# Kernel tuning notes

Hardware: AMD Instinct MI355X
Metric: run time of the kernel (lower is better)

The kernel has to match this reference:

```python
import jax, jax.numpy as jnp
import numpy as np

B, H, W, D = 32, 56, 56, 192
WS, NH, SHIFT = 7, 6, 3
DH = D // NH          # head dim = 32
N = WS * WS           # 49 tokens per window
NW = (H // WS) * (W // WS)  # 64 windows per image
EPS = 1e-5


def _rel_pos_index():
    coords = np.stack(np.meshgrid(np.arange(WS), np.arange(WS), indexing='ij'))  # (2,WS,WS)
    flat = coords.reshape(2, -1)
    rel = flat[:, :, None] - flat[:, None, :]            # (2,N,N)
    rel = rel.transpose(1, 2, 0).astype(np.int64)        # (N,N,2)
    rel[..., 0] += WS - 1
    rel[..., 1] += WS - 1
    rel[..., 0] *= 2 * WS - 1
    return rel.sum(-1)                                    # (N,N) in [0,169)


def _shift_mask():
    img = np.zeros((H, W))
    bounds = [(0, H - WS), (H - WS, H - SHIFT), (H - SHIFT, H)]
    cnt = 0
    for h0, h1 in bounds:
        for w0, w1 in bounds:
            img[h0:h1, w0:w1] = cnt
            cnt += 1
    win = img.reshape(H // WS, WS, W // WS, WS).transpose(0, 2, 1, 3).reshape(-1, N)  # (nW,N)
    diff = win[:, None, :] - win[:, :, None]
    return np.where(diff != 0, -100.0, 0.0).astype(np.float32)  # (nW,N,N)


_REL_IDX = jnp.asarray(_rel_pos_index())
_MASK = jnp.asarray(_shift_mask())


def _layernorm(x, g, b):
    mu = jnp.mean(x, -1, keepdims=True)
    var = jnp.mean(jnp.square(x - mu), -1, keepdims=True)
    return (x - mu) * jax.lax.rsqrt(var + EPS) * g + b


def _window_partition(x):  # (B,H,W,C) -> (B*nW, N, C)
    Bx, _, _, C = x.shape
    x = x.reshape(Bx, H // WS, WS, W // WS, WS, C).transpose(0, 1, 3, 2, 4, 5)
    return x.reshape(-1, N, C)


def _window_reverse(w):  # (B*nW, N, C) -> (B,H,W,C)
    C = w.shape[-1]
    x = w.reshape(-1, H // WS, W // WS, WS, WS, C).transpose(0, 1, 3, 2, 4, 5)
    return x.reshape(-1, H, W, C)


def setup_inputs() -> dict:
    key = jax.random.key(0)
    ks = jax.random.split(key, 8)
    s = 0.02
    return {
        'x': jax.random.normal(ks[0], (B, H * W, D), jnp.float32),
        'norm1_g': jnp.ones((D,), jnp.float32),
        'norm1_b': jnp.zeros((D,), jnp.float32),
        'qkv_w': jax.random.normal(ks[1], (D, 3 * D), jnp.float32) * s,
        'qkv_b': jnp.zeros((3 * D,), jnp.float32),
        'proj_wo': jax.random.normal(ks[2], (D, D), jnp.float32) * s,
        'proj_bo': jnp.zeros((D,), jnp.float32),
        'rpb': jax.random.normal(ks[3], ((2 * WS - 1) ** 2, NH), jnp.float32) * s,
        'pl_w': jax.random.normal(ks[4], (NH, NH), jnp.float32) * s,
        'pl_b': jnp.zeros((NH,), jnp.float32),
        'pw_w': jax.random.normal(ks[5], (NH, NH), jnp.float32) * s,
        'pw_b': jnp.zeros((NH,), jnp.float32),
        'norm2_g': jnp.ones((D,), jnp.float32),
        'norm2_b': jnp.zeros((D,), jnp.float32),
        'fc1_w': jax.random.normal(ks[6], (D, 4 * D), jnp.float32) * s,
        'fc1_b': jnp.zeros((4 * D,), jnp.float32),
        'fc2_w': jax.random.normal(ks[7], (4 * D, D), jnp.float32) * s,
        'fc2_b': jnp.zeros((D,), jnp.float32),
    }


def reference(x, norm1_g, norm1_b, qkv_w, qkv_b, proj_wo, proj_bo, rpb,
              pl_w, pl_b, pw_w, pw_b, norm2_g, norm2_b,
              fc1_w, fc1_b, fc2_w, fc2_b):
    shortcut = x
    h = _layernorm(x, norm1_g, norm1_b).reshape(B, H, W, D)
    h = jnp.roll(h, (-SHIFT, -SHIFT), (1, 2))             # shifted windows
    win = _window_partition(h)                            # (B_, N, D), B_ = B*NW
    B_ = win.shape[0]

    qkv = win @ qkv_w + qkv_b                             # (B_, N, 3D)
    q_out, k_out, v_out = qkv[..., :D], qkv[..., D:2 * D], qkv[..., 2 * D:]
    qkv5 = qkv.reshape(B_, N, 3, NH, DH)
    q = qkv5[:, :, 0].transpose(0, 2, 1, 3)               # (B_, H, N, d)
    k = qkv5[:, :, 1].transpose(0, 2, 1, 3)
    v = qkv5[:, :, 2].transpose(0, 2, 1, 3)

    scale = DH ** -0.5
    attn = jnp.einsum('bhnd,bhmd->bhnm', q * scale, k)    # (B_, H, N, N)
    bias = rpb[_REL_IDX.reshape(-1)].reshape(N, N, NH).transpose(2, 0, 1)
    attn = attn + bias[None]
    # proj_l over the head axis (distillation transform, pre-softmax)
    attn = jnp.einsum('bhnm,hg->bgnm', attn, pl_w) + pl_b[None, :, None, None]
    # shifted-window mask
    attn = attn.reshape(B, NW, NH, N, N) + _MASK[None, :, None]
    attn = jax.nn.softmax(attn.reshape(B_, NH, N, N), axis=-1)
    # proj_w over the head axis (post-softmax)
    attn = jnp.einsum('bhnm,hg->bgnm', attn, pw_w) + pw_b[None, :, None, None]

    out = jnp.einsum('bhnm,bhmd->bnhd', attn, v).reshape(B_, N, D)
    out = out @ proj_wo + proj_bo

    h = _window_reverse(out)                              # (B,H,W,D)
    h = jnp.roll(h, (SHIFT, SHIFT), (1, 2)).reshape(B, H * W, D)
    xo = shortcut + h

    m = _layernorm(xo, norm2_g, norm2_b)
    m = jax.nn.gelu(m @ fc1_w + fc1_b, approximate=False) @ fc2_w + fc2_b
    xo = xo + m
    return xo, (q_out, k_out, v_out)
```

## Files before the change

kernel.cpp:

```cpp
#include <hip/hip_runtime.h>
#include <math.h>

#define TOK   100352
#define OUTCH 19267584L
#define NWIN  2048

typedef __attribute__((ext_vector_type(4))) float f32x4;
typedef __attribute__((ext_vector_type(8))) short bf16x8;

__device__ __forceinline__ unsigned short f2bf(float f) {
    unsigned u = __builtin_bit_cast(unsigned, f);
    u += 0x7FFFu + ((u >> 16) & 1u);
    return (unsigned short)(u >> 16);
}
__device__ __forceinline__ float bf2f(unsigned short s) {
    return __builtin_bit_cast(float, (unsigned)s << 16);
}

__global__ __launch_bounds__(256) void k_prep_w(const float* __restrict__ qkv_w,
                                                const float* __restrict__ proj_w,
                                                const float* __restrict__ fc1_w,
                                                const float* __restrict__ fc2_w,
                                                unsigned short* __restrict__ wt)
{
    int i = blockIdx.x * 256 + threadIdx.x;
    float v;
    if (i < 110592) {
        int instr = i >> 9, rem = i & 511, lane = rem >> 3, j = rem & 7;
        int ks = instr % 6, t = instr / 6;
        int ni = t % 3, t2 = t / 3;
        int wv = t2 & 3, s = t2 >> 2;
        int n = s * 192 + wv * 48 + ni * 16 + (lane & 15);
        int k = ks * 32 + ((lane >> 4) << 3) + j;
        v = qkv_w[k * 576 + n];
    } else if (i < 147456) {
        int j2 = i - 110592;
        int instr = j2 >> 9, rem = j2 & 511, lane = rem >> 3, j = rem & 7;
        int ks = instr % 6, t = instr / 6;
        int ni = t & 1, hh = t >> 1;
        int n = hh * 32 + ni * 16 + (lane & 15);
        int k = ks * 32 + ((lane >> 4) << 3) + j;
        v = proj_w[k * 192 + n];
    } else if (i < 294912) {
        int j2 = i - 147456;
        int instr = j2 >> 9, rem = j2 & 511, lane = rem >> 3, j = rem & 7;
        int ks = instr % 6, t = instr / 6;
        int ni = t % 3, t2 = t / 3;
        int wv = t2 & 3, s = t2 >> 2;
        int n = s * 192 + wv * 48 + ni * 16 + (lane & 15);
        int k = ks * 32 + ((lane >> 4) << 3) + j;
        v = fc1_w[k * 768 + n];
    } else {
        int j2 = i - 294912;
        int instr = j2 >> 9, rem = j2 & 511, lane = rem >> 3, j = rem & 7;
        int ks = instr % 6, t = instr / 6;
        int ni = t % 3, t2 = t / 3;
        int wv = t2 & 3, s = t2 >> 2;
        int n = wv * 48 + ni * 16 + (lane & 15);
        int k = s * 192 + ks * 32 + ((lane >> 4) << 3) + j;
        v = fc2_w[k * 192 + n];
    }
    wt[i] = f2bf(v);
}

__global__ __launch_bounds__(256) void k_qkv(const float* __restrict__ x,
                                             const float* __restrict__ g,
                                             const float* __restrict__ b,
                                             const unsigned short* __restrict__ wp,
                                             const float* __restrict__ bias,
                                             float* __restrict__ outq)
{
    __shared__ unsigned short lA[64 * 192];
    const int tid = threadIdx.x, lane = tid & 63, wv = tid >> 6;
    const int s = blockIdx.x;
    const long m0 = (long)blockIdx.y * 64;

    {
        int r = tid >> 2, c0 = (tid & 3) * 48;
        int t = (int)m0 + r;
        int w = t / 49, n = t - w * 49;
        int bb = w >> 6, widx = w & 63;
        int wi = widx >> 3, wj = widx & 7;
        int rr = n / 7, ss = n - rr * 7;
        int hh = wi * 7 + rr + 3; if (hh >= 56) hh -= 56;
        int ww = wj * 7 + ss + 3; if (ww >= 56) ww -= 56;
        const f32x4* sp = (const f32x4*)(x + ((long)(bb * 56 + hh) * 56 + ww) * 192 + c0);
        f32x4 vv[12];
        float sum = 0.f, sq = 0.f;
        #pragma unroll
        for (int i = 0; i < 12; i++) {
            vv[i] = sp[i];
            #pragma unroll
            for (int j = 0; j < 4; j++) { sum += vv[i][j]; sq += vv[i][j] * vv[i][j]; }
        }
        sum += __shfl_xor(sum, 1); sq += __shfl_xor(sq, 1);
        sum += __shfl_xor(sum, 2); sq += __shfl_xor(sq, 2);
        float mu = sum * (1.f / 192.f);
        float rs = rsqrtf(sq * (1.f / 192.f) - mu * mu + 1e-5f);
        #pragma unroll
        for (int i = 0; i < 6; i++) {
            bf16x8 o8;
            #pragma unroll
            for (int j = 0; j < 8; j++) {
                int idx = i * 8 + j, c = c0 + idx;
                o8[j] = (short)f2bf((vv[idx >> 2][idx & 3] - mu) * rs * g[c] + b[c]);
            }
            *(bf16x8*)((char*)lA + r * 384 + ((2 * (c0 + i * 8)) ^ ((r & 7) << 4))) = o8;
        }
    }
    __syncthreads();

    f32x4 acc[4][3];
    #pragma unroll
    for (int mi = 0; mi < 4; mi++)
        #pragma unroll
        for (int ni = 0; ni < 3; ni++) acc[mi][ni] = (f32x4){0.f, 0.f, 0.f, 0.f};
    #pragma unroll
    for (int ks = 0; ks < 6; ks++) {
        int kb = ks * 64 + ((lane >> 4) << 4);
        bf16x8 bfr[3];
        #pragma unroll
        for (int ni = 0; ni < 3; ni++) {
            int instr = ((s * 4 + wv) * 3 + ni) * 6 + ks;
            bfr[ni] = *(const bf16x8*)(wp + (instr << 9) + (lane << 3));
        }
        #pragma unroll
        for (int mi = 0; mi < 4; mi++) {
            int row = mi * 16 + (lane & 15);
            bf16x8 afr = *(const bf16x8*)((char*)lA + row * 384 + (kb ^ ((row & 7) << 4)));
            #pragma unroll
            for (int ni = 0; ni < 3; ni++)
                acc[mi][ni] = __builtin_amdgcn_mfma_f32_16x16x32_bf16(afr, bfr[ni], acc[mi][ni], 0, 0, 0);
        }
    }

    #pragma unroll
    for (int mi = 0; mi < 4; mi++)
        #pragma unroll
        for (int ni = 0; ni < 3; ni++) {
            int gc = wv * 48 + ni * 16 + (lane & 15);
            float bv = bias[s * 192 + gc];
            #pragma unroll
            for (int r4 = 0; r4 < 4; r4++) {
                long lr = mi * 16 + ((lane >> 4) << 2) + r4;
                outq[(long)s * OUTCH + (m0 + lr) * 192 + gc] = acc[mi][ni][r4] + bv;
            }
        }
}

__global__ __launch_bounds__(256) void k_mlp(const unsigned short* __restrict__ h2,
                                             const unsigned short* __restrict__ w1p,
                                             const float* __restrict__ b1,
                                             const unsigned short* __restrict__ w2p,
                                             const float* __restrict__ b2,
                                             const unsigned short* __restrict__ xv,
                                             float* __restrict__ xo)
{
    __shared__ unsigned short lA[64 * 192];
    __shared__ unsigned short lH[64 * 192];
    const int tid = threadIdx.x, lane = tid & 63, wv = tid >> 6;
    const long m0 = (long)blockIdx.x * 64;

    #pragma unroll
    for (int c = tid; c < 64 * 24; c += 256) {
        int row = c / 24, k16 = c - row * 24;
        bf16x8 v = *(const bf16x8*)(h2 + (m0 + row) * 192 + k16 * 8);
        *(bf16x8*)((char*)lA + row * 384 + ((k16 * 16) ^ ((row & 7) << 4))) = v;
    }

    f32x4 acc2[4][3];
    #pragma unroll
    for (int mi = 0; mi < 4; mi++)
        #pragma unroll
        for (int ni = 0; ni < 3; ni++) acc2[mi][ni] = (f32x4){0.f, 0.f, 0.f, 0.f};
    __syncthreads();

    for (int s = 0; s < 4; s++) {
        f32x4 acc1[4][3];
        #pragma unroll
        for (int mi = 0; mi < 4; mi++)
            #pragma unroll
            for (int ni = 0; ni < 3; ni++) acc1[mi][ni] = (f32x4){0.f, 0.f, 0.f, 0.f};
        #pragma unroll
        for (int ks = 0; ks < 6; ks++) {
            int kb = ks * 64 + ((lane >> 4) << 4);
            bf16x8 bfr[3];
            #pragma unroll
            for (int ni = 0; ni < 3; ni++) {
                int instr = ((s * 4 + wv) * 3 + ni) * 6 + ks;
                bfr[ni] = *(const bf16x8*)(w1p + (instr << 9) + (lane << 3));
            }
            #pragma unroll
            for (int mi = 0; mi < 4; mi++) {
                int row = mi * 16 + (lane & 15);
                bf16x8 afr = *(const bf16x8*)((char*)lA + row * 384 + (kb ^ ((row & 7) << 4)));
                #pragma unroll
                for (int ni = 0; ni < 3; ni++)
                    acc1[mi][ni] = __builtin_amdgcn_mfma_f32_16x16x32_bf16(afr, bfr[ni], acc1[mi][ni], 0, 0, 0);
            }
        }
        __syncthreads();
        #pragma unroll
        for (int mi = 0; mi < 4; mi++)
            #pragma unroll
            for (int ni = 0; ni < 3; ni++) {
                int col = wv * 48 + ni * 16 + (lane & 15);
                float bv = b1[s * 192 + col];
                #pragma unroll
                for (int r = 0; r < 4; r++) {
                    int row = mi * 16 + ((lane >> 4) << 2) + r;
                    float v = acc1[mi][ni][r] + bv;
                    float ge = 0.5f * v * (1.f + erff(v * 0.70710678118654752f));
                    *(unsigned short*)((char*)lH + row * 384 + ((2 * col) ^ ((row & 7) << 4))) = f2bf(ge);
                }
            }
        __syncthreads();
        #pragma unroll
        for (int ks = 0; ks < 6; ks++) {
            int kb = ks * 64 + ((lane >> 4) << 4);
            bf16x8 bfr[3];
            #pragma unroll
            for (int ni = 0; ni < 3; ni++) {
                int instr = ((s * 4 + wv) * 3 + ni) * 6 + ks;
                bfr[ni] = *(const bf16x8*)(w2p + (instr << 9) + (lane << 3));
            }
            #pragma unroll
            for (int mi = 0; mi < 4; mi++) {
                int row = mi * 16 + (lane & 15);
                bf16x8 afr = *(const bf16x8*)((char*)lH + row * 384 + (kb ^ ((row & 7) << 4)));
                #pragma unroll
                for (int ni = 0; ni < 3; ni++)
                    acc2[mi][ni] = __builtin_amdgcn_mfma_f32_16x16x32_bf16(afr, bfr[ni], acc2[mi][ni], 0, 0, 0);
            }
        }
    }
    #pragma unroll
    for (int mi = 0; mi < 4; mi++)
        #pragma unroll
        for (int ni = 0; ni < 3; ni++) {
            int gcol = wv * 48 + ni * 16 + (lane & 15);
            float bv = b2[gcol];
            #pragma unroll
            for (int r = 0; r < 4; r++) {
                long grow = m0 + mi * 16 + ((lane >> 4) << 2) + r;
                xo[grow * 192 + gcol] = bf2f(xv[grow * 192 + gcol]) + acc2[mi][ni][r] + bv;
            }
        }
}

#define ATS 67
__global__ __launch_bounds__(384) void k_attn(const float* __restrict__ qg,
                                              const float* __restrict__ kg,
                                              const float* __restrict__ vg,
                                              const float* __restrict__ rpb,
                                              const float* __restrict__ plw,
                                              const float* __restrict__ plb,
                                              const float* __restrict__ pww,
                                              const float* __restrict__ pwb,
                                              const unsigned short* __restrict__ projp,
                                              const float* __restrict__ pbias,
                                              const float* __restrict__ x,
                                              const float* __restrict__ g2,
                                              const float* __restrict__ b2,
                                              unsigned short* __restrict__ xv,
                                              unsigned short* __restrict__ h2)
{
    __shared__ __align__(16) char SM[78800];
    float (*ATT)[49][ATS] = (float(*)[49][ATS])SM;
    float (*xoT)[196]     = (float(*)[196])(SM + 19200);

    int w = blockIdx.x, widx = w & 63;
    int tid = threadIdx.x, lane = tid & 63, h = tid >> 6;
    const long base = (long)w * 49 * 192;
    int wi = widx >> 3, wj = widx & 7, bb = w >> 6;

    bf16x8 vfr[2][2];
    #pragma unroll
    for (int kst = 0; kst < 2; kst++)
        #pragma unroll
        for (int ni = 0; ni < 2; ni++) {
            int d = ni * 16 + (lane & 15);
            #pragma unroll
            for (int j = 0; j < 8; j++) {
                int n = kst * 32 + ((lane >> 4) << 3) + j; if (n > 48) n = 48;
                vfr[kst][ni][j] = (short)f2bf(vg[base + n * 192 + h * 32 + d]);
            }
        }

    for (int c = tid; c < 6 * 49 * 15; c += 384) {
        int g = c / (49 * 15), rem = c - g * (49 * 15);
        int m = rem / 15, n = 49 + (rem - m * 15);
        ATT[g][m][n] = 0.f;
    }

    bf16x8 qfr[4], kfr[4];
    #pragma unroll
    for (int mi = 0; mi < 4; mi++) {
        int m = mi * 16 + (lane & 15); if (m > 48) m = 48;
        const float* qp = qg + base + m * 192 + h * 32 + ((lane >> 4) << 3);
        #pragma unroll
        for (int j = 0; j < 8; j++) qfr[mi][j] = (short)f2bf(qp[j]);
    }
    #pragma unroll
    for (int ni = 0; ni < 4; ni++) {
        int n = ni * 16 + (lane & 15); if (n > 48) n = 48;
        const float* kp = kg + base + n * 192 + h * 32 + ((lane >> 4) << 3);
        #pragma unroll
        for (int j = 0; j < 8; j++) kfr[ni][j] = (short)f2bf(kp[j]);
    }
    f32x4 sa[4][4];
    #pragma unroll
    for (int ni = 0; ni < 4; ni++)
        #pragma unroll
        for (int mi = 0; mi < 4; mi++)
            sa[mi][ni] = __builtin_amdgcn_mfma_f32_16x16x32_bf16(qfr[mi], kfr[ni], (f32x4){0.f, 0.f, 0.f, 0.f}, 0, 0, 0);
    const float scale = 0.17677669529663687f;
    #pragma unroll
    for (int mi = 0; mi < 4; mi++)
        #pragma unroll
        for (int ni = 0; ni < 4; ni++)
            #pragma unroll
            for (int r = 0; r < 4; r++) {
                int m = mi * 16 + ((lane >> 4) << 2) + r, n = ni * 16 + (lane & 15);
                if (m < 49 && n < 49) {
                    int rq = m / 7, cq = m - rq * 7, rk = n / 7, ck = n - rk * 7;
                    int ridx = (rq - rk + 6) * 13 + (cq - ck + 6);
                    ATT[h][m][n] = sa[mi][ni][r] * scale + rpb[ridx * 6 + h];
                }
            }
    __syncthreads();

    for (int p = tid; p < 2401; p += 384) {
        int m = p / 49, n = p - m * 49;
        float a[6];
        #pragma unroll
        for (int g = 0; g < 6; g++) a[g] = ATT[g][m][n];
        int rq = m / 7, cq = m - rq * 7, rk = n / 7, ck = n - rk * 7;
        int ghq = wi * 7 + rq, gwq = wj * 7 + cq, ghk = wi * 7 + rk, gwk = wj * 7 + ck;
        int regq = (ghq < 49 ? 0 : (ghq < 53 ? 1 : 2)) * 3 + (gwq < 49 ? 0 : (gwq < 53 ? 1 : 2));
        int regk = (ghk < 49 ? 0 : (ghk < 53 ? 1 : 2)) * 3 + (gwk < 49 ? 0 : (gwk < 53 ? 1 : 2));
        float msk = (regq != regk) ? -100.f : 0.f;
        #pragma unroll
        for (int g = 0; g < 6; g++) {
            float v = plb[g] + msk;
            #pragma unroll
            for (int h2i = 0; h2i < 6; h2i++) v += a[h2i] * plw[h2i * 6 + g];
            ATT[g][m][n] = v;
        }
    }
    __syncthreads();

    if (tid < 294) {
        int g = tid / 49, m = tid - g * 49;
        float* row = &ATT[g][m][0];
        float mx = row[0];
        #pragma unroll
        for (int j = 1; j < 49; j++) mx = fmaxf(mx, row[j]);
        float e[49]; float sm = 0.f;
        #pragma unroll
        for (int j = 0; j < 49; j++) { e[j] = __expf(row[j] - mx); sm += e[j]; }
        float inv = 1.f / sm;
        #pragma unroll
        for (int j = 0; j < 49; j++) row[j] = e[j] * inv;
    }
    __syncthreads();

    for (int p = tid; p < 2401; p += 384) {
        int m = p / 49, n = p - m * 49;
        float a[6];
        #pragma unroll
        for (int g = 0; g < 6; g++) a[g] = ATT[g][m][n];
        #pragma unroll
        for (int g = 0; g < 6; g++) {
            float v = pwb[g];
            #pragma unroll
            for (int h2i = 0; h2i < 6; h2i++) v += a[h2i] * pww[h2i * 6 + g];
            ATT[g][m][n] = v;
        }
    }
    __syncthreads();

    f32x4 oa[4][2];
    #pragma unroll
    for (int mi = 0; mi < 4; mi++)
        #pragma unroll
        for (int ni = 0; ni < 2; ni++) oa[mi][ni] = (f32x4){0.f, 0.f, 0.f, 0.f};
    #pragma unroll
    for (int kst = 0; kst < 2; kst++) {
        #pragma unroll
        for (int mi = 0; mi < 4; mi++) {
            int m = mi * 16 + (lane & 15); if (m > 48) m = 48;
            const float* ap = &ATT[h][m][kst * 32 + ((lane >> 4) << 3)];
            bf16x8 afr;
            #pragma unroll
            for (int j = 0; j < 8; j++) afr[j] = (short)f2bf(ap[j]);
            #pragma unroll
            for (int ni = 0; ni < 2; ni++)
                oa[mi][ni] = __builtin_amdgcn_mfma_f32_16x16x32_bf16(afr, vfr[kst][ni], oa[mi][ni], 0, 0, 0);
        }
    }
    __syncthreads();

    #pragma unroll
    for (int mi = 0; mi < 4; mi++)
        #pragma unroll
        for (int ni = 0; ni < 2; ni++)
            #pragma unroll
            for (int r = 0; r < 4; r++) {
                int m = mi * 16 + ((lane >> 4) << 2) + r;
                if (m < 49) {
                    int col = h * 32 + ni * 16 + (lane & 15);
                    *(unsigned short*)(SM + m * 384 + ((2 * col) ^ ((m & 7) << 4))) = f2bf(oa[mi][ni][r]);
                }
            }
    __syncthreads();

    f32x4 pacc[4][2];
    #pragma unroll
    for (int mi = 0; mi < 4; mi++)
        #pragma unroll
        for (int ni = 0; ni < 2; ni++) pacc[mi][ni] = (f32x4){0.f, 0.f, 0.f, 0.f};
    #pragma unroll
    for (int ks = 0; ks < 6; ks++) {
        int kb = ks * 64 + ((lane >> 4) << 4);
        bf16x8 bfr[2];
        #pragma unroll
        for (int ni = 0; ni < 2; ni++) {
            int instr = (h * 2 + ni) * 6 + ks;
            bfr[ni] = *(const bf16x8*)(projp + (instr << 9) + (lane << 3));
        }
        #pragma unroll
        for (int mi = 0; mi < 4; mi++) {
            int row = mi * 16 + (lane & 15); if (row > 48) row = 48;
            bf16x8 afr = *(const bf16x8*)(SM + row * 384 + (kb ^ ((row & 7) << 4)));
            #pragma unroll
            for (int ni = 0; ni < 2; ni++)
                pacc[mi][ni] = __builtin_amdgcn_mfma_f32_16x16x32_bf16(afr, bfr[ni], pacc[mi][ni], 0, 0, 0);
        }
    }

    #pragma unroll
    for (int mi = 0; mi < 4; mi++)
        #pragma unroll
        for (int ni = 0; ni < 2; ni++) {
            int gc = h * 32 + ni * 16 + (lane & 15);
            float bv = pbias[gc];
            #pragma unroll
            for (int r = 0; r < 4; r++) {
                int m = mi * 16 + ((lane >> 4) << 2) + r;
                if (m < 49) {
                    int rr = m / 7, ss = m - rr * 7;
                    int ho = wi * 7 + rr + 3; if (ho >= 56) ho -= 56;
                    int wo = wj * 7 + ss + 3; if (wo >= 56) wo -= 56;
                    long tp = ((long)(bb * 56 + ho) * 56 + wo);
                    xoT[m][gc] = x[tp * 192 + gc] + pacc[mi][ni][r] + bv;
                }
            }
        }
    __syncthreads();

    if (tid < 196) {
        int m = tid >> 2, c0 = (tid & 3) * 48;
        float vv[48];
        float sum = 0.f, sq = 0.f;
        #pragma unroll
        for (int i = 0; i < 48; i++) { vv[i] = xoT[m][c0 + i]; sum += vv[i]; sq += vv[i] * vv[i]; }
        sum += __shfl_xor(sum, 1); sq += __shfl_xor(sq, 1);
        sum += __shfl_xor(sum, 2); sq += __shfl_xor(sq, 2);
        float mu = sum * (1.f / 192.f);
        float rs = rsqrtf(sq * (1.f / 192.f) - mu * mu + 1e-5f);
        int rr = m / 7, ss = m - rr * 7;
        int ho = wi * 7 + rr + 3; if (ho >= 56) ho -= 56;
        int wo = wj * 7 + ss + 3; if (wo >= 56) wo -= 56;
        long tp = ((long)(bb * 56 + ho) * 56 + wo);
        #pragma unroll
        for (int i = 0; i < 6; i++) {
            bf16x8 o8, x8;
            #pragma unroll
            for (int j = 0; j < 8; j++) {
                int c = c0 + i * 8 + j;
                float xvf = vv[i * 8 + j];
                x8[j] = (short)f2bf(xvf);
                o8[j] = (short)f2bf((xvf - mu) * rs * g2[c] + b2[c]);
            }
            *(bf16x8*)(h2 + tp * 192 + c0 + i * 8) = o8;
            *(bf16x8*)(xv + tp * 192 + c0 + i * 8) = x8;
        }
    }
}

extern "C" void kernel_launch(void* const* d_in, const int* in_sizes, int n_in,
                              void* d_out, int out_size, void* d_ws, size_t ws_size,
                              hipStream_t stream)
{
    const float* x      = (const float*)d_in[0];
    const float* n1g    = (const float*)d_in[1];
    const float* n1b    = (const float*)d_in[2];
    const float* qkv_w  = (const float*)d_in[3];
    const float* qkv_b  = (const float*)d_in[4];
    const float* proj_w = (const float*)d_in[5];
    const float* proj_b = (const float*)d_in[6];
    const float* rpb    = (const float*)d_in[7];
    const float* pl_w   = (const float*)d_in[8];
    const float* pl_b   = (const float*)d_in[9];
    const float* pw_w   = (const float*)d_in[10];
    const float* pw_b   = (const float*)d_in[11];
    const float* n2g    = (const float*)d_in[12];
    const float* n2b    = (const float*)d_in[13];
    const float* fc1_w  = (const float*)d_in[14];
    const float* fc1_b  = (const float*)d_in[15];
    const float* fc2_w  = (const float*)d_in[16];
    const float* fc2_b  = (const float*)d_in[17];

    float* out   = (float*)d_out;
    float* out_q = out + OUTCH;
    float* out_k = out + 2 * OUTCH;
    float* out_v = out + 3 * OUTCH;

    char* ws = (char*)d_ws;
    unsigned short* bufT = (unsigned short*)ws;
    unsigned short* xvB  = (unsigned short*)(ws + 38535168);
    unsigned short* bufW = (unsigned short*)(ws + 2 * 38535168L);

    k_prep_w<<<1728, 256, 0, stream>>>(qkv_w, proj_w, fc1_w, fc2_w, bufW);
    k_qkv<<<dim3(3, 1568), 256, 0, stream>>>(x, n1g, n1b, bufW, qkv_b, out_q);
    k_attn<<<NWIN, 384, 0, stream>>>(out_q, out_k, out_v,
                                     rpb, pl_w, pl_b, pw_w, pw_b,
                                     bufW + 110592, proj_b, x, n2g, n2b,
                                     xvB, bufT);
    k_mlp<<<1568, 256, 0, stream>>>(bufT, bufW + 147456, fc1_b, bufW + 294912, fc2_b,
                                    xvB, out);
}
```

Baseline: 459.7 us.

## Fuse LayerNorm and QKV projection into the window attention kernel

```diff
diff --git a/kernel.cpp b/kernel.cpp
--- a/kernel.cpp
+++ b/kernel.cpp
@@ -28,9 +28,9 @@
     if (i < 110592) {
         int instr = i >> 9, rem = i & 511, lane = rem >> 3, j = rem & 7;
         int ks = instr % 6, t = instr / 6;
-        int ni = t % 3, t2 = t / 3;
-        int wv = t2 & 3, s = t2 >> 2;
-        int n = s * 192 + wv * 48 + ni * 16 + (lane & 15);
+        int ni = t & 1, t2 = t >> 1;
+        int hh = t2 % 6, s = t2 / 6;
+        int n = s * 192 + hh * 32 + ni * 16 + (lane & 15);
         int k = ks * 32 + ((lane >> 4) << 3) + j;
         v = qkv_w[k * 576 + n];
     } else if (i < 147456) {
@@ -63,91 +63,6 @@
     wt[i] = f2bf(v);
 }
 
-__global__ __launch_bounds__(256) void k_qkv(const float* __restrict__ x,
-                                             const float* __restrict__ g,
-                                             const float* __restrict__ b,
-                                             const unsigned short* __restrict__ wp,
-                                             const float* __restrict__ bias,
-                                             float* __restrict__ outq)
-{
-    __shared__ unsigned short lA[64 * 192];
-    const int tid = threadIdx.x, lane = tid & 63, wv = tid >> 6;
-    const int s = blockIdx.x;
-    const long m0 = (long)blockIdx.y * 64;
-
-    {
-        int r = tid >> 2, c0 = (tid & 3) * 48;
-        int t = (int)m0 + r;
-        int w = t / 49, n = t - w * 49;
-        int bb = w >> 6, widx = w & 63;
-        int wi = widx >> 3, wj = widx & 7;
-        int rr = n / 7, ss = n - rr * 7;
-        int hh = wi * 7 + rr + 3; if (hh >= 56) hh -= 56;
-        int ww = wj * 7 + ss + 3; if (ww >= 56) ww -= 56;
-        const f32x4* sp = (const f32x4*)(x + ((long)(bb * 56 + hh) * 56 + ww) * 192 + c0);
-        f32x4 vv[12];
-        float sum = 0.f, sq = 0.f;
-        #pragma unroll
-        for (int i = 0; i < 12; i++) {
-            vv[i] = sp[i];
-            #pragma unroll
-            for (int j = 0; j < 4; j++) { sum += vv[i][j]; sq += vv[i][j] * vv[i][j]; }
-        }
-        sum += __shfl_xor(sum, 1); sq += __shfl_xor(sq, 1);
-        sum += __shfl_xor(sum, 2); sq += __shfl_xor(sq, 2);
-        float mu = sum * (1.f / 192.f);
-        float rs = rsqrtf(sq * (1.f / 192.f) - mu * mu + 1e-5f);
-        #pragma unroll
-        for (int i = 0; i < 6; i++) {
-            bf16x8 o8;
-            #pragma unroll
-            for (int j = 0; j < 8; j++) {
-                int idx = i * 8 + j, c = c0 + idx;
-                o8[j] = (short)f2bf((vv[idx >> 2][idx & 3] - mu) * rs * g[c] + b[c]);
-            }
-            *(bf16x8*)((char*)lA + r * 384 + ((2 * (c0 + i * 8)) ^ ((r & 7) << 4))) = o8;
-        }
-    }
-    __syncthreads();
-
-    f32x4 acc[4][3];
-    #pragma unroll
-    for (int mi = 0; mi < 4; mi++)
-        #pragma unroll
-        for (int ni = 0; ni < 3; ni++) acc[mi][ni] = (f32x4){0.f, 0.f, 0.f, 0.f};
-    #pragma unroll
-    for (int ks = 0; ks < 6; ks++) {
-        int kb = ks * 64 + ((lane >> 4) << 4);
-        bf16x8 bfr[3];
-        #pragma unroll
-        for (int ni = 0; ni < 3; ni++) {
-            int instr = ((s * 4 + wv) * 3 + ni) * 6 + ks;
-            bfr[ni] = *(const bf16x8*)(wp + (instr << 9) + (lane << 3));
-        }
-        #pragma unroll
-        for (int mi = 0; mi < 4; mi++) {
-            int row = mi * 16 + (lane & 15);
-            bf16x8 afr = *(const bf16x8*)((char*)lA + row * 384 + (kb ^ ((row & 7) << 4)));
-            #pragma unroll
-            for (int ni = 0; ni < 3; ni++)
-                acc[mi][ni] = __builtin_amdgcn_mfma_f32_16x16x32_bf16(afr, bfr[ni], acc[mi][ni], 0, 0, 0);
-        }
-    }
-
-    #pragma unroll
-    for (int mi = 0; mi < 4; mi++)
-        #pragma unroll
-        for (int ni = 0; ni < 3; ni++) {
-            int gc = wv * 48 + ni * 16 + (lane & 15);
-            float bv = bias[s * 192 + gc];
-            #pragma unroll
-            for (int r4 = 0; r4 < 4; r4++) {
-                long lr = mi * 16 + ((lane >> 4) << 2) + r4;
-                outq[(long)s * OUTCH + (m0 + lr) * 192 + gc] = acc[mi][ni][r4] + bv;
-            }
-        }
-}
-
 __global__ __launch_bounds__(256) void k_mlp(const unsigned short* __restrict__ h2,
                                              const unsigned short* __restrict__ w1p,
                                              const float* __restrict__ b1,
@@ -249,9 +164,14 @@
 }
 
 #define ATS 67
-__global__ __launch_bounds__(384) void k_attn(const float* __restrict__ qg,
-                                              const float* __restrict__ kg,
-                                              const float* __restrict__ vg,
+#define QL_OFF 78800
+#define KL_OFF 97616
+#define VL_OFF 116432
+__global__ __launch_bounds__(384) void k_attn(const float* __restrict__ x,
+                                              const float* __restrict__ n1g,
+                                              const float* __restrict__ n1b,
+                                              const unsigned short* __restrict__ qkvp,
+                                              const float* __restrict__ qbias,
                                               const float* __restrict__ rpb,
                                               const float* __restrict__ plw,
                                               const float* __restrict__ plb,
@@ -259,33 +179,110 @@
                                               const float* __restrict__ pwb,
                                               const unsigned short* __restrict__ projp,
                                               const float* __restrict__ pbias,
-                                              const float* __restrict__ x,
                                               const float* __restrict__ g2,
                                               const float* __restrict__ b2,
+                                              float* __restrict__ outq,
                                               unsigned short* __restrict__ xv,
                                               unsigned short* __restrict__ h2)
 {
-    __shared__ __align__(16) char SM[78800];
+    __shared__ __align__(16) char SM[136240];
     float (*ATT)[49][ATS] = (float(*)[49][ATS])SM;
     float (*xoT)[196]     = (float(*)[196])(SM + 19200);
 
     int w = blockIdx.x, widx = w & 63;
     int tid = threadIdx.x, lane = tid & 63, h = tid >> 6;
-    const long base = (long)w * 49 * 192;
     int wi = widx >> 3, wj = widx & 7, bb = w >> 6;
-
-    bf16x8 vfr[2][2];
-    #pragma unroll
-    for (int kst = 0; kst < 2; kst++)
+    const long rowbase = (long)w * 49;
+    const bool bdry = (wi == 7) || (wj == 7);
+
+    if (tid < 196) {
+        int r = tid >> 2, c0 = (tid & 3) * 48;
+        int rr = r / 7, ss = r - rr * 7;
+        int hh = wi * 7 + rr + 3; if (hh >= 56) hh -= 56;
+        int ww = wj * 7 + ss + 3; if (ww >= 56) ww -= 56;
+        const f32x4* sp = (const f32x4*)(x + ((long)(bb * 56 + hh) * 56 + ww) * 192 + c0);
+        f32x4 vv[12];
+        float sum = 0.f, sq = 0.f;
+        #pragma unroll
+        for (int i = 0; i < 12; i++) {
+            vv[i] = sp[i];
+            #pragma unroll
+            for (int j = 0; j < 4; j++) { sum += vv[i][j]; sq += vv[i][j] * vv[i][j]; }
+        }
+        sum += __shfl_xor(sum, 1); sq += __shfl_xor(sq, 1);
+        sum += __shfl_xor(sum, 2); sq += __shfl_xor(sq, 2);
+        float mu = sum * (1.f / 192.f);
+        float rs = rsqrtf(sq * (1.f / 192.f) - mu * mu + 1e-5f);
+        #pragma unroll
+        for (int i = 0; i < 6; i++) {
+            bf16x8 o8;
+            #pragma unroll
+            for (int j = 0; j < 8; j++) {
+                int idx = i * 8 + j, c = c0 + idx;
+                o8[j] = (short)f2bf((vv[idx >> 2][idx & 3] - mu) * rs * n1g[c] + n1b[c]);
+            }
+            *(bf16x8*)(SM + r * 384 + ((2 * (c0 + i * 8)) ^ ((r & 7) << 4))) = o8;
+        }
+    }
+    __syncthreads();
+
+    f32x4 aq[4][2], ak[4][2], av[4][2];
+    #pragma unroll
+    for (int mi = 0; mi < 4; mi++)
         #pragma unroll
         for (int ni = 0; ni < 2; ni++) {
-            int d = ni * 16 + (lane & 15);
-            #pragma unroll
-            for (int j = 0; j < 8; j++) {
-                int n = kst * 32 + ((lane >> 4) << 3) + j; if (n > 48) n = 48;
-                vfr[kst][ni][j] = (short)f2bf(vg[base + n * 192 + h * 32 + d]);
-            }
-        }
+            aq[mi][ni] = (f32x4){0.f, 0.f, 0.f, 0.f};
+            ak[mi][ni] = (f32x4){0.f, 0.f, 0.f, 0.f};
+            av[mi][ni] = (f32x4){0.f, 0.f, 0.f, 0.f};
+        }
+    #pragma unroll
+    for (int ks = 0; ks < 6; ks++) {
+        int kb = ks * 64 + ((lane >> 4) << 4);
+        bf16x8 afr[4];
+        #pragma unroll
+        for (int mi = 0; mi < 4; mi++) {
+            int row = mi * 16 + (lane & 15);
+            afr[mi] = *(const bf16x8*)(SM + row * 384 + (kb ^ ((row & 7) << 4)));
+        }
+        bf16x8 bq[2], bk[2], bv[2];
+        #pragma unroll
+        for (int ni = 0; ni < 2; ni++) {
+            bq[ni] = *(const bf16x8*)(qkvp + (((((0 * 6 + h) * 2 + ni) * 6 + ks)) << 9) + (lane << 3));
+            bk[ni] = *(const bf16x8*)(qkvp + (((((1 * 6 + h) * 2 + ni) * 6 + ks)) << 9) + (lane << 3));
+            bv[ni] = *(const bf16x8*)(qkvp + (((((2 * 6 + h) * 2 + ni) * 6 + ks)) << 9) + (lane << 3));
+        }
+        #pragma unroll
+        for (int mi = 0; mi < 4; mi++)
+            #pragma unroll
+            for (int ni = 0; ni < 2; ni++) {
+                aq[mi][ni] = __builtin_amdgcn_mfma_f32_16x16x32_bf16(afr[mi], bq[ni], aq[mi][ni], 0, 0, 0);
+                ak[mi][ni] = __builtin_amdgcn_mfma_f32_16x16x32_bf16(afr[mi], bk[ni], ak[mi][ni], 0, 0, 0);
+                av[mi][ni] = __builtin_amdgcn_mfma_f32_16x16x32_bf16(afr[mi], bv[ni], av[mi][ni], 0, 0, 0);
+            }
+    }
+    #pragma unroll
+    for (int mi = 0; mi < 4; mi++)
+        #pragma unroll
+        for (int ni = 0; ni < 2; ni++) {
+            int col = h * 32 + ni * 16 + (lane & 15);
+            float bgq = qbias[col], bgk = qbias[192 + col], bgv = qbias[384 + col];
+            #pragma unroll
+            for (int r = 0; r < 4; r++) {
+                int m = mi * 16 + ((lane >> 4) << 2) + r;
+                if (m < 49) {
+                    long gr = (rowbase + m) * 192 + col;
+                    float fq = aq[mi][ni][r] + bgq;
+                    float fk = ak[mi][ni][r] + bgk;
+                    float fv = av[mi][ni][r] + bgv;
+                    outq[gr] = fq; outq[OUTCH + gr] = fk; outq[2 * OUTCH + gr] = fv;
+                    int sw = (2 * col) ^ ((m & 7) << 4);
+                    *(unsigned short*)(SM + QL_OFF + m * 384 + sw) = f2bf(fq);
+                    *(unsigned short*)(SM + KL_OFF + m * 384 + sw) = f2bf(fk);
+                    *(unsigned short*)(SM + VL_OFF + m * 404 + 2 * col) = f2bf(fv);
+                }
+            }
+        }
+    __syncthreads();
 
     for (int c = tid; c < 6 * 49 * 15; c += 384) {
         int g = c / (49 * 15), rem = c - g * (49 * 15);
@@ -297,16 +294,12 @@
     #pragma unroll
     for (int mi = 0; mi < 4; mi++) {
         int m = mi * 16 + (lane & 15); if (m > 48) m = 48;
-        const float* qp = qg + base + m * 192 + h * 32 + ((lane >> 4) << 3);
-        #pragma unroll
-        for (int j = 0; j < 8; j++) qfr[mi][j] = (short)f2bf(qp[j]);
+        qfr[mi] = *(const bf16x8*)(SM + QL_OFF + m * 384 + ((h * 64 + ((lane >> 4) << 4)) ^ ((m & 7) << 4)));
     }
     #pragma unroll
     for (int ni = 0; ni < 4; ni++) {
         int n = ni * 16 + (lane & 15); if (n > 48) n = 48;
-        const float* kp = kg + base + n * 192 + h * 32 + ((lane >> 4) << 3);
-        #pragma unroll
-        for (int j = 0; j < 8; j++) kfr[ni][j] = (short)f2bf(kp[j]);
+        kfr[ni] = *(const bf16x8*)(SM + KL_OFF + n * 384 + ((h * 64 + ((lane >> 4) << 4)) ^ ((n & 7) << 4)));
     }
     f32x4 sa[4][4];
     #pragma unroll
@@ -335,11 +328,14 @@
         float a[6];
         #pragma unroll
         for (int g = 0; g < 6; g++) a[g] = ATT[g][m][n];
-        int rq = m / 7, cq = m - rq * 7, rk = n / 7, ck = n - rk * 7;
-        int ghq = wi * 7 + rq, gwq = wj * 7 + cq, ghk = wi * 7 + rk, gwk = wj * 7 + ck;
-        int regq = (ghq < 49 ? 0 : (ghq < 53 ? 1 : 2)) * 3 + (gwq < 49 ? 0 : (gwq < 53 ? 1 : 2));
-        int regk = (ghk < 49 ? 0 : (ghk < 53 ? 1 : 2)) * 3 + (gwk < 49 ? 0 : (gwk < 53 ? 1 : 2));
-        float msk = (regq != regk) ? -100.f : 0.f;
+        float msk = 0.f;
+        if (bdry) {
+            int rq = m / 7, cq = m - rq * 7, rk = n / 7, ck = n - rk * 7;
+            int ghq = wi * 7 + rq, gwq = wj * 7 + cq, ghk = wi * 7 + rk, gwk = wj * 7 + ck;
+            int regq = (ghq < 49 ? 0 : (ghq < 53 ? 1 : 2)) * 3 + (gwq < 49 ? 0 : (gwq < 53 ? 1 : 2));
+            int regk = (ghk < 49 ? 0 : (ghk < 53 ? 1 : 2)) * 3 + (gwk < 49 ? 0 : (gwk < 53 ? 1 : 2));
+            msk = (regq != regk) ? -100.f : 0.f;
+        }
         #pragma unroll
         for (int g = 0; g < 6; g++) {
             float v = plb[g] + msk;
@@ -380,6 +376,18 @@
     }
     __syncthreads();
 
+    bf16x8 vfr[2][2];
+    #pragma unroll
+    for (int kst = 0; kst < 2; kst++)
+        #pragma unroll
+        for (int ni = 0; ni < 2; ni++) {
+            int d = h * 32 + ni * 16 + (lane & 15);
+            #pragma unroll
+            for (int j = 0; j < 8; j++) {
+                int n = kst * 32 + ((lane >> 4) << 3) + j; if (n > 48) n = 48;
+                vfr[kst][ni][j] = *(const unsigned short*)(SM + VL_OFF + n * 404 + 2 * d);
+            }
+        }
     f32x4 oa[4][2];
     #pragma unroll
     for (int mi = 0; mi < 4; mi++)
@@ -514,8 +522,6 @@
 
     float* out   = (float*)d_out;
     float* out_q = out + OUTCH;
-    float* out_k = out + 2 * OUTCH;
-    float* out_v = out + 3 * OUTCH;
 
     char* ws = (char*)d_ws;
     unsigned short* bufT = (unsigned short*)ws;
@@ -523,11 +529,10 @@
     unsigned short* bufW = (unsigned short*)(ws + 2 * 38535168L);
 
     k_prep_w<<<1728, 256, 0, stream>>>(qkv_w, proj_w, fc1_w, fc2_w, bufW);
-    k_qkv<<<dim3(3, 1568), 256, 0, stream>>>(x, n1g, n1b, bufW, qkv_b, out_q);
-    k_attn<<<NWIN, 384, 0, stream>>>(out_q, out_k, out_v,
+    k_attn<<<NWIN, 384, 0, stream>>>(x, n1g, n1b, bufW, qkv_b,
                                      rpb, pl_w, pl_b, pw_w, pw_b,
-                                     bufW + 110592, proj_b, x, n2g, n2b,
-                                     xvB, bufT);
+                                     bufW + 110592, proj_b, n2g, n2b,
+                                     out_q, xvB, bufT);
     k_mlp<<<1568, 256, 0, stream>>>(bufT, bufW + 147456, fc1_b, bufW + 294912, fc2_b,
                                     xvB, out);
 }
```

New measurement: 397.3 us (median of 2 runs). 13.6% less time.
